# Performance work log

Hardware: AMD Instinct MI355X
Metric: run time of the kernel (lower is better)

Reference implementation:

```python
import jax, jax.numpy as jnp
import numpy as np
from jax import lax

QBITS = 8  # per layer_configs: 8-bit weights and activations


def fake_quant(x, bits=QBITS):
    """Per-tensor symmetric fake quantization with straight-through estimator."""
    qmax = float(2 ** (bits - 1) - 1)  # 127 for 8-bit
    scale = jnp.maximum(jnp.max(jnp.abs(x)), 1e-8) / qmax
    q = jnp.clip(jnp.round(x / scale), -qmax - 1.0, qmax) * scale
    # STE: forward uses q, backward passes gradient through unchanged
    return x + lax.stop_gradient(q - x)


def qconv(x, w, b):
    """Fake-quantized conv: quantize activations and weights, then VALID conv + bias."""
    xq = fake_quant(x)
    wq = fake_quant(w)
    y = lax.conv_general_dilated(
        xq, wq, window_strides=(1, 1), padding='VALID',
        dimension_numbers=('NCHW', 'OIHW', 'NCHW'))
    return y + b[None, :, None, None]


def setup_inputs() -> dict:
    key = jax.random.key(0)
    ks = jax.random.split(key, 9)
    return {
        'x':  jax.random.uniform(ks[0], (256, 1, 128, 128), dtype=jnp.float32),
        'w1': jax.random.normal(ks[1], (16, 1, 3, 3), dtype=jnp.float32) * 0.3,
        'b1': jax.random.normal(ks[2], (16,), dtype=jnp.float32) * 0.05,
        'w2': jax.random.normal(ks[3], (16, 16, 3, 3), dtype=jnp.float32) * 0.1,
        'b2': jax.random.normal(ks[4], (16,), dtype=jnp.float32) * 0.05,
        'w3': jax.random.normal(ks[5], (16, 16, 3, 3), dtype=jnp.float32) * 0.1,
        'b3': jax.random.normal(ks[6], (16,), dtype=jnp.float32) * 0.05,
        'w4': jax.random.normal(ks[7], (1, 16, 2, 2), dtype=jnp.float32) * 0.1,
        'b4': jax.random.normal(ks[8], (1,), dtype=jnp.float32) * 0.05,
    }


def reference(x, w1, b1, w2, b2, w3, b3, w4, b4):
    # x: [N,1,128,128] -> [N,16,126,126] -> [N,16,124,124] -> [N,16,122,122] -> [N,1,121,121]
    h = jax.nn.relu(qconv(x, w1, b1))
    h = jax.nn.relu(qconv(h, w2, b2))
    h = jax.nn.relu(qconv(h, w3, b3))
    return jax.nn.sigmoid(qconv(h, w4, b4))
```

## Files before the change

### kernel.cpp

```cpp
#include <hip/hip_runtime.h>
#include <math.h>


#define THREADS 256

typedef __attribute__((ext_vector_type(4))) int i32x4;

__device__ __forceinline__ int xcd_swz(int bid, int nwg) {
    return (bid & 7) * (nwg >> 3) + (bid >> 3);
}

__device__ __forceinline__ int swzb(int rec) {
    return (rec << 4) ^ ((rec & 56) << 1);
}

__device__ __forceinline__ float block_reduce_max(float m, float* wred) {
#pragma unroll
    for (int off = 32; off > 0; off >>= 1)
        m = fmaxf(m, __shfl_down(m, off, 64));
    if ((threadIdx.x & 63) == 0) wred[threadIdx.x >> 6] = m;
    __syncthreads();
    return fmaxf(fmaxf(wred[0], wred[1]), fmaxf(wred[2], wred[3]));
}

__global__ void init_kernel(unsigned int* slots) {
    if (threadIdx.x < 8) slots[threadIdx.x] = 0u;
}

__global__ void fill_kernel(float* out, int n, float v) {
    int i = blockIdx.x * blockDim.x + threadIdx.x;
    int stride = gridDim.x * blockDim.x;
    for (; i < n; i += stride) out[i] = v;
}

__global__ __launch_bounds__(THREADS) void absmax4_kernel(
    const float4* __restrict__ x, int n4, unsigned int* __restrict__ slot) {
    __shared__ float wred[4];
    float m = 0.f;
    const int stride = gridDim.x * blockDim.x;
    for (int i = blockIdx.x * blockDim.x + threadIdx.x; i < n4; i += stride) {
        float4 v = x[i];
        m = fmaxf(fmaxf(fabsf(v.x), fabsf(v.y)),
                  fmaxf(fmaxf(fabsf(v.z), fabsf(v.w)), m));
    }
    m = block_reduce_max(m, wred);
    if (threadIdx.x == 0) atomicMax(slot, __float_as_uint(m));
}

__global__ __launch_bounds__(THREADS) void quant_w_kernel(
    const float* __restrict__ w1, const float* __restrict__ w2,
    const float* __restrict__ w3, const float* __restrict__ w4,
    float* __restrict__ qw1, float* __restrict__ qw4,
    signed char* __restrict__ wi8_2, signed char* __restrict__ wi8_3,
    unsigned int* __restrict__ slots) {
    __shared__ float wred[4];
    const float* w; int nel;
    switch (blockIdx.x) {
        case 0:  w = w1; nel = 144;  break;
        case 1:  w = w2; nel = 2304; break;
        case 2:  w = w3; nel = 2304; break;
        default: w = w4; nel = 64;   break;
    }
    float m = 0.f;
    for (int i = threadIdx.x; i < nel; i += blockDim.x)
        m = fmaxf(m, fabsf(w[i]));
    m = block_reduce_max(m, wred);
    if (threadIdx.x == 0) slots[4 + blockIdx.x] = __float_as_uint(m);
    const float s = fmaxf(m, 1e-8f) / 127.0f;

    if (blockIdx.x == 0) {
        for (int i = threadIdx.x; i < 144; i += blockDim.x) {
            int p = i % 9, o = i / 9;
            float q = fminf(fmaxf(rintf(w[i] / s), -128.f), 127.f);
            qw1[p * 16 + o] = q * s;
        }
    } else if (blockIdx.x == 3) {
        for (int i = threadIdx.x; i < 64; i += blockDim.x) {
            float q = fminf(fmaxf(rintf(w[i] / s), -128.f), 127.f);
            qw4[i] = q * s;
        }
    } else {
        signed char* wi8 = (blockIdx.x == 1) ? wi8_2 : wi8_3;
        for (int i = threadIdx.x; i < 3072; i += blockDim.x) {
            int ci = i & 15, lane = (i >> 4) & 63, g = i >> 10;
            int co = lane & 15, qq = lane >> 4;
            int pos = 4 * g + qq;
            float v = 0.f;
            if (pos < 9) {
                int ky = pos / 3, kx = pos % 3;
                v = fminf(fmaxf(rintf(w[((co * 16 + ci) * 3 + ky) * 3 + kx] / s),
                                -128.f), 127.f);
            }
            wi8[i] = (signed char)(int)v;
        }
    }
}

template <int MODE>
__global__ __launch_bounds__(THREADS) void conv1_kernel(
    const float* __restrict__ x, const float* __restrict__ qw,
    const float* __restrict__ bias, signed char* __restrict__ out,
    unsigned int* __restrict__ slots) {
    constexpr int IH = 128, IW = 128, OH = 126, OW = 126;
    __shared__ float tile[34 * 34];
    __shared__ float wred[4];
    const int bid = xcd_swz(blockIdx.x, gridDim.x);
    const int n = bid >> 4, tr = bid & 15;
    const int oy0 = (tr >> 2) * 32, ox0 = (tr & 3) * 32;
    const float s_in = fmaxf(__uint_as_float(slots[0]), 1e-8f) / 127.0f;
    const float* xN = x + (size_t)n * IH * IW;

#pragma unroll
    for (int it = 0; it < 5; ++it) {
        int px = it * 256 + threadIdx.x;
        if (px < 1156) {
            int iy = px / 34, ix = px - iy * 34;
            int gy = min(oy0 + iy, IH - 1), gx = min(ox0 + ix, IW - 1);
            float q = rintf(xN[gy * IW + gx] / s_in);
            tile[px] = fminf(fmaxf(q, -128.f), 127.f);
        }
    }
    __syncthreads();

    const int tx = (threadIdx.x & 15) * 2, ty = (threadIdx.x >> 4) * 2;

    float p[4][4];
#pragma unroll
    for (int r = 0; r < 4; ++r) {
        const float* rp = &tile[(ty + r) * 34 + tx];
        p[r][0] = rp[0]; p[r][1] = rp[1]; p[r][2] = rp[2]; p[r][3] = rp[3];
    }

    float r_out = 0.f;
    if constexpr (MODE == 2)
        r_out = 127.0f / fmaxf(__uint_as_float(slots[1]), 1e-8f);

    float accm[16];
#pragma unroll
    for (int c = 0; c < 16; ++c) accm[c] = -3.0e38f;

#pragma unroll
    for (int sy = 0; sy < 2; ++sy)
#pragma unroll
    for (int sx = 0; sx < 2; ++sx) {
        float acc[16];
#pragma unroll
        for (int c = 0; c < 16; ++c) acc[c] = 0.f;
#pragma unroll
        for (int ky = 0; ky < 3; ++ky)
#pragma unroll
        for (int kx = 0; kx < 3; ++kx) {
            const float xv = p[sy + ky][sx + kx];
            const float* wp = qw + (ky * 3 + kx) * 16;
#pragma unroll
            for (int co = 0; co < 16; ++co)
                acc[co] = fmaf(xv, wp[co], acc[co]);
        }
        const int oy = oy0 + ty + sy, ox = ox0 + tx + sx;
        const bool ok = (oy < OH) && (ox < OW);
        if constexpr (MODE == 1) {
            if (ok) {
#pragma unroll
                for (int co = 0; co < 16; ++co)
                    accm[co] = fmaxf(accm[co], acc[co]);
            }
        } else {
            unsigned pk[4] = {0u, 0u, 0u, 0u};
#pragma unroll
            for (int co = 0; co < 16; ++co) {
                float y = fmaxf(fmaf(acc[co], s_in, bias[co]), 0.f);
                float q8 = fminf(rintf(y * r_out), 127.f);
                pk[co >> 2] |= ((unsigned)(int)q8) << ((co & 3) * 8);
            }
            if (ok) {
                int4 v; v.x = pk[0]; v.y = pk[1]; v.z = pk[2]; v.w = pk[3];
                *(int4*)(out + ((size_t)(n * OH + oy) * OW + ox) * 16) = v;
            }
        }
    }
    if constexpr (MODE == 1) {
        float m = 0.f;
#pragma unroll
        for (int co = 0; co < 16; ++co)
            m = fmaxf(m, fmaxf(fmaf(accm[co], s_in, bias[co]), 0.f));
        m = block_reduce_max(m, wred);
        if (threadIdx.x == 0) atomicMax(&slots[1], __float_as_uint(m));
    }
}

template <bool STORE>
__global__ __launch_bounds__(THREADS) void mconv_kernel(
    const signed char* __restrict__ in, const signed char* __restrict__ wi8,
    const float* __restrict__ bias, signed char* __restrict__ out,
    unsigned int* __restrict__ slots, int in_slot, int w_slot, int out_slot,
    int IH, int IW) {
    __shared__ signed char tile[1156 * 16 + 128];
    __shared__ float wred[4];
    const int OH = IH - 2, OW = IW - 2;
    const int bid = xcd_swz(blockIdx.x, gridDim.x);
    const int n = bid >> 4, tr = bid & 15;
    const int oy0 = (tr >> 2) * 32, ox0 = (tr & 3) * 32;

    const int tid = threadIdx.x, lane = tid & 63, wv = tid >> 6;
    const int q = lane >> 4, col = lane & 15;

    const signed char* inN = in + (size_t)n * IH * IW * 16;

#pragma unroll
    for (int it = 0; it < 5; ++it) {
        int px = it * 256 + tid;
        if (px < 1156) {
            int iy = px / 34, ix = px - iy * 34;
            int gy = min(oy0 + iy, IH - 1), gx = min(ox0 + ix, IW - 1);
            *(int4*)(tile + swzb(px)) =
                *(const int4*)(inN + ((size_t)gy * IW + gx) * 16);
        }
    }

    i32x4 afrag[3];
#pragma unroll
    for (int g = 0; g < 3; ++g)
        afrag[g] = ((const i32x4*)wi8)[g * 64 + lane];

    __syncthreads();

    int drec[3];
#pragma unroll
    for (int g = 0; g < 3; ++g) {
        int pos = 4 * g + q;
        int dy = (pos < 9) ? pos / 3 : 0;
        int dx = (pos < 9) ? pos % 3 : 0;
        drec[g] = dy * 34 + dx;
    }
    const int wr = wv >> 1, wc = wv & 1;
    const int bx = 16 * wc + col;
    const int ox = ox0 + bx;

    const float s_in = fmaxf(__uint_as_float(slots[in_slot]), 1e-8f) / 127.0f;
    const float s_w  = fmaxf(__uint_as_float(slots[w_slot]),  1e-8f) / 127.0f;
    const float sxw = s_in * s_w;
    float bj[4];
#pragma unroll
    for (int j = 0; j < 4; ++j) bj[j] = bias[q * 4 + j];
    float r_out = 0.f;
    if constexpr (STORE)
        r_out = 127.0f / fmaxf(__uint_as_float(slots[out_slot]), 1e-8f);

    signed char* outN = out + (size_t)n * OH * OW * 16;
    int mi[4];
#pragma unroll
    for (int j = 0; j < 4; ++j) mi[j] = INT_MIN;

#pragma unroll 4
    for (int r = 0; r < 16; ++r) {
        const int iy = 16 * wr + r;
        const int rec = iy * 34 + bx;
        i32x4 acc = {0, 0, 0, 0};
#pragma unroll
        for (int g = 0; g < 3; ++g) {
            i32x4 b = *(const i32x4*)(tile + swzb(rec + drec[g]));
            acc = __builtin_amdgcn_mfma_i32_16x16x64_i8(afrag[g], b, acc, 0, 0, 0);
        }
        const int oy = oy0 + iy;
        const bool ok = (oy < OH) && (ox < OW);
        if constexpr (STORE) {
            unsigned pk = 0u;
#pragma unroll
            for (int j = 0; j < 4; ++j) {
                float y = fmaxf(fmaf((float)acc[j], sxw, bj[j]), 0.f);
                float q8 = fminf(rintf(y * r_out), 127.f);
                pk |= ((unsigned)(int)q8) << (j * 8);
            }
            if (ok)
                *(unsigned*)(outN + ((size_t)oy * OW + ox) * 16 + q * 4) = pk;
        } else {
            if (ok) {
#pragma unroll
                for (int j = 0; j < 4; ++j)
                    mi[j] = (acc[j] > mi[j]) ? acc[j] : mi[j];
            }
        }
    }
    if constexpr (!STORE) {
        float m = 0.f;
#pragma unroll
        for (int j = 0; j < 4; ++j)
            m = fmaxf(m, fmaxf(fmaf((float)mi[j], sxw, bj[j]), 0.f));
        m = block_reduce_max(m, wred);
        if (tid == 0) atomicMax(&slots[out_slot], __float_as_uint(m));
    }
}

__global__ __launch_bounds__(THREADS) void conv4_kernel(
    const signed char* __restrict__ in, const float* __restrict__ qw,
    const float* __restrict__ bias, float* __restrict__ out,
    unsigned int* __restrict__ slots) {
    constexpr int IH = 122, IW = 122, OH = 121, OW = 121;
    const int bid = xcd_swz(blockIdx.x, gridDim.x);
    const int n = bid >> 4, tr = bid & 15;
    const int oyb = (tr >> 2) * 32 + ((threadIdx.x >> 4) * 2);
    const int oxb = (tr & 3) * 32 + ((threadIdx.x & 15) * 2);
    const float s_in = fmaxf(__uint_as_float(slots[3]), 1e-8f) / 127.0f;
    const float b0 = bias[0];
    const signed char* inN = in + (size_t)n * IH * IW * 16;

    float w[64];
#pragma unroll
    for (int i = 0; i < 64; ++i) w[i] = qw[i];

#pragma unroll
    for (int sy = 0; sy < 2; ++sy)
#pragma unroll
    for (int sx = 0; sx < 2; ++sx) {
        const int oy = oyb + sy, ox = oxb + sx;
        if (oy >= OH || ox >= OW) continue;
        float acc = 0.f;
#pragma unroll
        for (int ky = 0; ky < 2; ++ky)
#pragma unroll
        for (int kx = 0; kx < 2; ++kx) {
            union { int4 v; signed char c[16]; } u;
            u.v = *(const int4*)(inN + ((size_t)(oy + ky) * IW + ox + kx) * 16);
#pragma unroll
            for (int ci = 0; ci < 16; ++ci)
                acc = fmaf((float)u.c[ci], w[(ci * 2 + ky) * 2 + kx], acc);
        }
        float y = fmaf(acc, s_in, b0);
        out[(size_t)(n * OH + oy) * OW + ox] = 1.0f / (1.0f + expf(-y));
    }
}

extern "C" void kernel_launch(void* const* d_in, const int* in_sizes, int n_in,
                              void* d_out, int out_size, void* d_ws, size_t ws_size,
                              hipStream_t stream) {
    (void)in_sizes; (void)n_in;
    const float* x  = (const float*)d_in[0];
    const float* w1 = (const float*)d_in[1];
    const float* b1 = (const float*)d_in[2];
    const float* w2 = (const float*)d_in[3];
    const float* b2 = (const float*)d_in[4];
    const float* w3 = (const float*)d_in[5];
    const float* b3 = (const float*)d_in[6];
    const float* w4 = (const float*)d_in[7];
    const float* b4 = (const float*)d_in[8];

    char* ws = (char*)d_ws;
    unsigned int* slots = (unsigned int*)ws;
    float* qw1 = (float*)(ws + 256);
    float* qw4 = (float*)(ws + 1024);
    signed char* wi8_2 = (signed char*)(ws + 2048);
    signed char* wi8_3 = (signed char*)(ws + 5120);

    const size_t Q1 = 65028096ULL;
    const size_t Q2 = 62980096ULL;
    signed char* qb1 = (signed char*)(ws + 32768);
    signed char* qb2 = (signed char*)(ws + 32768 + Q1);
    float* outp = (float*)d_out;

    const size_t need = 32768ULL + Q1 + Q2;
    if (ws_size < need) {
        float v = 100.0f + (float)(ws_size >> 20);
        hipLaunchKernelGGL(fill_kernel, dim3(1024), dim3(THREADS), 0, stream,
                           outp, out_size, v);
        return;
    }

    const int blocks = 256 * 16;

    hipLaunchKernelGGL(init_kernel, dim3(1), dim3(64), 0, stream, slots);
    hipLaunchKernelGGL(absmax4_kernel, dim3(2048), dim3(THREADS), 0, stream,
                       (const float4*)x, 256 * 128 * 128 / 4, slots + 0);
    hipLaunchKernelGGL(quant_w_kernel, dim3(4), dim3(THREADS), 0, stream,
                       w1, w2, w3, w4, qw1, qw4, wi8_2, wi8_3, slots);

    hipLaunchKernelGGL((conv1_kernel<1>), dim3(blocks), dim3(THREADS), 0, stream,
                       x, qw1, b1, nullptr, slots);
    hipLaunchKernelGGL((conv1_kernel<2>), dim3(blocks), dim3(THREADS), 0, stream,
                       x, qw1, b1, qb1, slots);
    hipLaunchKernelGGL((mconv_kernel<false>), dim3(blocks), dim3(THREADS), 0, stream,
                       qb1, wi8_2, b2, nullptr, slots, 1, 5, 2, 126, 126);
    hipLaunchKernelGGL((mconv_kernel<true>), dim3(blocks), dim3(THREADS), 0, stream,
                       qb1, wi8_2, b2, qb2, slots, 1, 5, 2, 126, 126);
    hipLaunchKernelGGL((mconv_kernel<false>), dim3(blocks), dim3(THREADS), 0, stream,
                       qb2, wi8_3, b3, nullptr, slots, 2, 6, 3, 124, 124);
    hipLaunchKernelGGL((mconv_kernel<true>), dim3(blocks), dim3(THREADS), 0, stream,
                       qb2, wi8_3, b3, qb1, slots, 2, 6, 3, 124, 124);
    hipLaunchKernelGGL(conv4_kernel, dim3(blocks), dim3(THREADS), 0, stream,
                       qb1, qw4, b4, outp, slots);
}
```

Measured before the change: 333.5 us.

## Fuse adjacent conv stages with halo tiles to cut kernel launches and intermediate traffic

Replaces the seven-pass schedule (a max pass and a store pass per layer) with four kernels. Each kernel computes one layer's quantized output into shared memory and immediately runs the next layer's max-reduction or convolution on it. Tiles shrink to 30x30 outputs with overlapping halos, giving 25 tiles per image. This removes several full reads of the int8 intermediates and the separate conv4 pass. In exchange, halo work is recomputed, shared memory per block grows, and fewer blocks may fit per CU.

```diff
diff --git a/kernel.cpp b/kernel.cpp
--- a/kernel.cpp
+++ b/kernel.cpp
@@ -9,7 +9,6 @@
 __device__ __forceinline__ int xcd_swz(int bid, int nwg) {
     return (bid & 7) * (nwg >> 3) + (bid >> 3);
 }
-
 __device__ __forceinline__ int swzb(int rec) {
     return (rec << 4) ^ ((rec & 56) << 1);
 }
@@ -96,11 +95,9 @@
     }
 }
 
-template <int MODE>
-__global__ __launch_bounds__(THREADS) void conv1_kernel(
+__global__ __launch_bounds__(THREADS) void conv1max_kernel(
     const float* __restrict__ x, const float* __restrict__ qw,
-    const float* __restrict__ bias, signed char* __restrict__ out,
-    unsigned int* __restrict__ slots) {
+    const float* __restrict__ bias, unsigned int* __restrict__ slots) {
     constexpr int IH = 128, IW = 128, OH = 126, OW = 126;
     __shared__ float tile[34 * 34];
     __shared__ float wred[4];
@@ -123,18 +120,12 @@
     __syncthreads();
 
     const int tx = (threadIdx.x & 15) * 2, ty = (threadIdx.x >> 4) * 2;
-
     float p[4][4];
 #pragma unroll
     for (int r = 0; r < 4; ++r) {
         const float* rp = &tile[(ty + r) * 34 + tx];
         p[r][0] = rp[0]; p[r][1] = rp[1]; p[r][2] = rp[2]; p[r][3] = rp[3];
     }
-
-    float r_out = 0.f;
-    if constexpr (MODE == 2)
-        r_out = 127.0f / fmaxf(__uint_as_float(slots[1]), 1e-8f);
-
     float accm[16];
 #pragma unroll
     for (int c = 0; c < 16; ++c) accm[c] = -3.0e38f;
@@ -157,73 +148,83 @@
                 acc[co] = fmaf(xv, wp[co], acc[co]);
         }
         const int oy = oy0 + ty + sy, ox = ox0 + tx + sx;
-        const bool ok = (oy < OH) && (ox < OW);
-        if constexpr (MODE == 1) {
-            if (ok) {
-#pragma unroll
-                for (int co = 0; co < 16; ++co)
-                    accm[co] = fmaxf(accm[co], acc[co]);
-            }
-        } else {
-            unsigned pk[4] = {0u, 0u, 0u, 0u};
-#pragma unroll
-            for (int co = 0; co < 16; ++co) {
-                float y = fmaxf(fmaf(acc[co], s_in, bias[co]), 0.f);
-                float q8 = fminf(rintf(y * r_out), 127.f);
-                pk[co >> 2] |= ((unsigned)(int)q8) << ((co & 3) * 8);
-            }
-            if (ok) {
-                int4 v; v.x = pk[0]; v.y = pk[1]; v.z = pk[2]; v.w = pk[3];
-                *(int4*)(out + ((size_t)(n * OH + oy) * OW + ox) * 16) = v;
-            }
-        }
-    }
-    if constexpr (MODE == 1) {
-        float m = 0.f;
-#pragma unroll
-        for (int co = 0; co < 16; ++co)
-            m = fmaxf(m, fmaxf(fmaf(accm[co], s_in, bias[co]), 0.f));
-        m = block_reduce_max(m, wred);
-        if (threadIdx.x == 0) atomicMax(&slots[1], __float_as_uint(m));
-    }
-}
-
-template <bool STORE>
-__global__ __launch_bounds__(THREADS) void mconv_kernel(
-    const signed char* __restrict__ in, const signed char* __restrict__ wi8,
-    const float* __restrict__ bias, signed char* __restrict__ out,
-    unsigned int* __restrict__ slots, int in_slot, int w_slot, int out_slot,
-    int IH, int IW) {
-    __shared__ signed char tile[1156 * 16 + 128];
+        if (oy < OH && ox < OW) {
+#pragma unroll
+            for (int co = 0; co < 16; ++co)
+                accm[co] = fmaxf(accm[co], acc[co]);
+        }
+    }
+    float m = 0.f;
+#pragma unroll
+    for (int co = 0; co < 16; ++co)
+        m = fmaxf(m, fmaxf(fmaf(accm[co], s_in, bias[co]), 0.f));
+    m = block_reduce_max(m, wred);
+    if (threadIdx.x == 0) atomicMax(&slots[1], __float_as_uint(m));
+}
+
+__global__ __launch_bounds__(THREADS) void k3_kernel(
+    const float* __restrict__ x, const float* __restrict__ qw1,
+    const float* __restrict__ b1, signed char* __restrict__ h1out,
+    const signed char* __restrict__ wi8_2, const float* __restrict__ b2,
+    unsigned int* __restrict__ slots) {
+    __shared__ float xt[36 * 36];
+    __shared__ signed char h1t[34 * 34 * 16 + 128];
     __shared__ float wred[4];
-    const int OH = IH - 2, OW = IW - 2;
     const int bid = xcd_swz(blockIdx.x, gridDim.x);
-    const int n = bid >> 4, tr = bid & 15;
-    const int oy0 = (tr >> 2) * 32, ox0 = (tr & 3) * 32;
-
-    const int tid = threadIdx.x, lane = tid & 63, wv = tid >> 6;
+    const int n = bid / 25, tr = bid % 25;
+    const int ty = (tr / 5) * 30, tx = (tr % 5) * 30;
+    const int tid = threadIdx.x;
+
+    const float s_x = fmaxf(__uint_as_float(slots[0]), 1e-8f) / 127.0f;
+    const float r1  = 127.0f / fmaxf(__uint_as_float(slots[1]), 1e-8f);
+    const float* xN = x + (size_t)n * 128 * 128;
+
+    for (int i = tid; i < 1296; i += THREADS) {
+        int iy = i / 36, ix = i - iy * 36;
+        int gy = min(ty + iy, 127), gx = min(tx + ix, 127);
+        float q = rintf(xN[gy * 128 + gx] / s_x);
+        xt[i] = fminf(fmaxf(q, -128.f), 127.f);
+    }
+    __syncthreads();
+
+    for (int p = tid; p < 1156; p += THREADS) {
+        int py = p / 34, px = p - py * 34;
+        float acc[16];
+#pragma unroll
+        for (int c = 0; c < 16; ++c) acc[c] = 0.f;
+#pragma unroll
+        for (int ky = 0; ky < 3; ++ky)
+#pragma unroll
+        for (int kx = 0; kx < 3; ++kx) {
+            const float xv = xt[(py + ky) * 36 + px + kx];
+            const float* wp = qw1 + (ky * 3 + kx) * 16;
+#pragma unroll
+            for (int co = 0; co < 16; ++co)
+                acc[co] = fmaf(xv, wp[co], acc[co]);
+        }
+        unsigned pk[4] = {0u, 0u, 0u, 0u};
+#pragma unroll
+        for (int co = 0; co < 16; ++co) {
+            float y = fmaxf(fmaf(acc[co], s_x, b1[co]), 0.f);
+            float q8 = fminf(rintf(y * r1), 127.f);
+            pk[co >> 2] |= ((unsigned)(int)q8) << ((co & 3) * 8);
+        }
+        int4 v; v.x = pk[0]; v.y = pk[1]; v.z = pk[2]; v.w = pk[3];
+        *(int4*)(h1t + swzb(p)) = v;
+        const int gy = ty + py, gx = tx + px;
+        if (gy <= 125 && gx <= 125)
+            *(int4*)(h1out + ((size_t)(n * 126 + gy) * 126 + gx) * 16) = v;
+    }
+
+    i32x4 afrag[3];
+#pragma unroll
+    for (int g = 0; g < 3; ++g)
+        afrag[g] = ((const i32x4*)wi8_2)[g * 64 + (tid & 63)];
+    __syncthreads();
+
+    const int lane = tid & 63, wv = tid >> 6;
     const int q = lane >> 4, col = lane & 15;
-
-    const signed char* inN = in + (size_t)n * IH * IW * 16;
-
-#pragma unroll
-    for (int it = 0; it < 5; ++it) {
-        int px = it * 256 + tid;
-        if (px < 1156) {
-            int iy = px / 34, ix = px - iy * 34;
-            int gy = min(oy0 + iy, IH - 1), gx = min(ox0 + ix, IW - 1);
-            *(int4*)(tile + swzb(px)) =
-                *(const int4*)(inN + ((size_t)gy * IW + gx) * 16);
-        }
-    }
-
-    i32x4 afrag[3];
-#pragma unroll
-    for (int g = 0; g < 3; ++g)
-        afrag[g] = ((const i32x4*)wi8)[g * 64 + lane];
-
-    __syncthreads();
-
+    const int wr = wv >> 1, wc = wv & 1;
     int drec[3];
 #pragma unroll
     for (int g = 0; g < 3; ++g) {
@@ -232,101 +233,246 @@
         int dx = (pos < 9) ? pos % 3 : 0;
         drec[g] = dy * 34 + dx;
     }
-    const int wr = wv >> 1, wc = wv & 1;
-    const int bx = 16 * wc + col;
-    const int ox = ox0 + bx;
-
-    const float s_in = fmaxf(__uint_as_float(slots[in_slot]), 1e-8f) / 127.0f;
-    const float s_w  = fmaxf(__uint_as_float(slots[w_slot]),  1e-8f) / 127.0f;
-    const float sxw = s_in * s_w;
-    float bj[4];
-#pragma unroll
-    for (int j = 0; j < 4; ++j) bj[j] = bias[q * 4 + j];
-    float r_out = 0.f;
-    if constexpr (STORE)
-        r_out = 127.0f / fmaxf(__uint_as_float(slots[out_slot]), 1e-8f);
-
-    signed char* outN = out + (size_t)n * OH * OW * 16;
+    const int ix2 = 16 * wc + col;
     int mi[4];
 #pragma unroll
     for (int j = 0; j < 4; ++j) mi[j] = INT_MIN;
 
 #pragma unroll 4
     for (int r = 0; r < 16; ++r) {
-        const int iy = 16 * wr + r;
-        const int rec = iy * 34 + bx;
+        const int iy2 = 16 * wr + r;
+        const int rec = iy2 * 34 + ix2;
         i32x4 acc = {0, 0, 0, 0};
 #pragma unroll
         for (int g = 0; g < 3; ++g) {
-            i32x4 b = *(const i32x4*)(tile + swzb(rec + drec[g]));
+            i32x4 b = *(const i32x4*)(h1t + swzb(rec + drec[g]));
             acc = __builtin_amdgcn_mfma_i32_16x16x64_i8(afrag[g], b, acc, 0, 0, 0);
         }
-        const int oy = oy0 + iy;
-        const bool ok = (oy < OH) && (ox < OW);
-        if constexpr (STORE) {
-            unsigned pk = 0u;
-#pragma unroll
-            for (int j = 0; j < 4; ++j) {
-                float y = fmaxf(fmaf((float)acc[j], sxw, bj[j]), 0.f);
-                float q8 = fminf(rintf(y * r_out), 127.f);
-                pk |= ((unsigned)(int)q8) << (j * 8);
+        if (ty + iy2 <= 123 && tx + ix2 <= 123) {
+#pragma unroll
+            for (int j = 0; j < 4; ++j)
+                mi[j] = (acc[j] > mi[j]) ? acc[j] : mi[j];
+        }
+    }
+    const float s1  = fmaxf(__uint_as_float(slots[1]), 1e-8f) / 127.0f;
+    const float sw2 = fmaxf(__uint_as_float(slots[5]), 1e-8f) / 127.0f;
+    const float sxw = s1 * sw2;
+    float m = 0.f;
+#pragma unroll
+    for (int j = 0; j < 4; ++j)
+        m = fmaxf(m, fmaxf(fmaf((float)mi[j], sxw, b2[q * 4 + j]), 0.f));
+    m = block_reduce_max(m, wred);
+    if (tid == 0) atomicMax(&slots[2], __float_as_uint(m));
+}
+
+__global__ __launch_bounds__(THREADS) void k4_kernel(
+    const signed char* __restrict__ h1, const signed char* __restrict__ wi8_2,
+    const float* __restrict__ b2, signed char* __restrict__ h2out,
+    const signed char* __restrict__ wi8_3, const float* __restrict__ b3,
+    unsigned int* __restrict__ slots) {
+    __shared__ signed char h1t[34 * 34 * 16 + 128];
+    __shared__ signed char h2t[32 * 32 * 16 + 128];
+    __shared__ float wred[4];
+    const int bid = xcd_swz(blockIdx.x, gridDim.x);
+    const int n = bid / 25, tr = bid % 25;
+    const int ty = (tr / 5) * 30, tx = (tr % 5) * 30;
+    const int tid = threadIdx.x, lane = tid & 63, wv = tid >> 6;
+    const int q = lane >> 4, col = lane & 15;
+    const int wr = wv >> 1, wc = wv & 1;
+
+    const signed char* h1N = h1 + (size_t)n * 126 * 126 * 16;
+#pragma unroll
+    for (int it = 0; it < 5; ++it) {
+        int p = it * 256 + tid;
+        if (p < 1156) {
+            int iy = p / 34, ix = p - iy * 34;
+            int gy = min(ty + iy, 125), gx = min(tx + ix, 125);
+            *(int4*)(h1t + swzb(p)) =
+                *(const int4*)(h1N + ((size_t)gy * 126 + gx) * 16);
+        }
+    }
+    i32x4 af2[3], af3[3];
+#pragma unroll
+    for (int g = 0; g < 3; ++g) {
+        af2[g] = ((const i32x4*)wi8_2)[g * 64 + lane];
+        af3[g] = ((const i32x4*)wi8_3)[g * 64 + lane];
+    }
+    __syncthreads();
+
+    int d34[3], d32[3];
+#pragma unroll
+    for (int g = 0; g < 3; ++g) {
+        int pos = 4 * g + q;
+        int dy = (pos < 9) ? pos / 3 : 0;
+        int dx = (pos < 9) ? pos % 3 : 0;
+        d34[g] = dy * 34 + dx;
+        d32[g] = dy * 32 + dx;
+    }
+    const float s1  = fmaxf(__uint_as_float(slots[1]), 1e-8f) / 127.0f;
+    const float sw2 = fmaxf(__uint_as_float(slots[5]), 1e-8f) / 127.0f;
+    const float sxw2 = s1 * sw2;
+    const float r2 = 127.0f / fmaxf(__uint_as_float(slots[2]), 1e-8f);
+    float b2j[4];
+#pragma unroll
+    for (int j = 0; j < 4; ++j) b2j[j] = b2[q * 4 + j];
+
+    const int ix2 = 16 * wc + col;
+    signed char* h2N = h2out + (size_t)n * 124 * 124 * 16;
+
+#pragma unroll 4
+    for (int r = 0; r < 16; ++r) {
+        const int iy2 = 16 * wr + r;
+        const int rec = iy2 * 34 + ix2;
+        i32x4 acc = {0, 0, 0, 0};
+#pragma unroll
+        for (int g = 0; g < 3; ++g) {
+            i32x4 b = *(const i32x4*)(h1t + swzb(rec + d34[g]));
+            acc = __builtin_amdgcn_mfma_i32_16x16x64_i8(af2[g], b, acc, 0, 0, 0);
+        }
+        unsigned pk = 0u;
+#pragma unroll
+        for (int j = 0; j < 4; ++j) {
+            float y = fmaxf(fmaf((float)acc[j], sxw2, b2j[j]), 0.f);
+            float q8 = fminf(rintf(y * r2), 127.f);
+            pk |= ((unsigned)(int)q8) << (j * 8);
+        }
+        *(unsigned*)(h2t + swzb(iy2 * 32 + ix2) + q * 4) = pk;
+        const int gy = ty + iy2, gx = tx + ix2;
+        if (gy <= 123 && gx <= 123)
+            *(unsigned*)(h2N + ((size_t)gy * 124 + gx) * 16 + q * 4) = pk;
+    }
+    __syncthreads();
+
+    int mi[4];
+#pragma unroll
+    for (int j = 0; j < 4; ++j) mi[j] = INT_MIN;
+#pragma unroll 4
+    for (int r = 0; r < 16; ++r) {
+        const int iy3 = 16 * wr + r;
+        if (iy3 <= 29) {
+            const int rec = iy3 * 32 + ix2;
+            i32x4 acc = {0, 0, 0, 0};
+#pragma unroll
+            for (int g = 0; g < 3; ++g) {
+                i32x4 b = *(const i32x4*)(h2t + swzb(rec + d32[g]));
+                acc = __builtin_amdgcn_mfma_i32_16x16x64_i8(af3[g], b, acc, 0, 0, 0);
             }
-            if (ok)
-                *(unsigned*)(outN + ((size_t)oy * OW + ox) * 16 + q * 4) = pk;
-        } else {
-            if (ok) {
+            if (ix2 <= 29 && ty + iy3 <= 121 && tx + ix2 <= 121) {
 #pragma unroll
                 for (int j = 0; j < 4; ++j)
                     mi[j] = (acc[j] > mi[j]) ? acc[j] : mi[j];
             }
         }
     }
-    if constexpr (!STORE) {
-        float m = 0.f;
-#pragma unroll
-        for (int j = 0; j < 4; ++j)
-            m = fmaxf(m, fmaxf(fmaf((float)mi[j], sxw, bj[j]), 0.f));
-        m = block_reduce_max(m, wred);
-        if (tid == 0) atomicMax(&slots[out_slot], __float_as_uint(m));
-    }
-}
-
-__global__ __launch_bounds__(THREADS) void conv4_kernel(
-    const signed char* __restrict__ in, const float* __restrict__ qw,
-    const float* __restrict__ bias, float* __restrict__ out,
+    const float s2  = fmaxf(__uint_as_float(slots[2]), 1e-8f) / 127.0f;
+    const float sw3 = fmaxf(__uint_as_float(slots[6]), 1e-8f) / 127.0f;
+    const float sxw3 = s2 * sw3;
+    float m = 0.f;
+#pragma unroll
+    for (int j = 0; j < 4; ++j)
+        m = fmaxf(m, fmaxf(fmaf((float)mi[j], sxw3, b3[q * 4 + j]), 0.f));
+    m = block_reduce_max(m, wred);
+    if (tid == 0) atomicMax(&slots[3], __float_as_uint(m));
+}
+
+__global__ __launch_bounds__(THREADS) void k5_kernel(
+    const signed char* __restrict__ h2, const signed char* __restrict__ wi8_3,
+    const float* __restrict__ b3, const float* __restrict__ qw4,
+    const float* __restrict__ b4, float* __restrict__ out,
     unsigned int* __restrict__ slots) {
-    constexpr int IH = 122, IW = 122, OH = 121, OW = 121;
+    __shared__ signed char h2t[34 * 34 * 16 + 128];
+    __shared__ signed char h3t[32 * 32 * 16 + 128];
     const int bid = xcd_swz(blockIdx.x, gridDim.x);
-    const int n = bid >> 4, tr = bid & 15;
-    const int oyb = (tr >> 2) * 32 + ((threadIdx.x >> 4) * 2);
-    const int oxb = (tr & 3) * 32 + ((threadIdx.x & 15) * 2);
-    const float s_in = fmaxf(__uint_as_float(slots[3]), 1e-8f) / 127.0f;
-    const float b0 = bias[0];
-    const signed char* inN = in + (size_t)n * IH * IW * 16;
-
+    const int n = bid / 25, tr = bid % 25;
+    const int ty = (tr / 5) * 30, tx = (tr % 5) * 30;
+    const int tid = threadIdx.x, lane = tid & 63, wv = tid >> 6;
+    const int q = lane >> 4, col = lane & 15;
+    const int wr = wv >> 1, wc = wv & 1;
+
+    const signed char* h2N = h2 + (size_t)n * 124 * 124 * 16;
+#pragma unroll
+    for (int it = 0; it < 5; ++it) {
+        int p = it * 256 + tid;
+        if (p < 1156) {
+            int iy = p / 34, ix = p - iy * 34;
+            int gy = min(ty + iy, 123), gx = min(tx + ix, 123);
+            *(int4*)(h2t + swzb(p)) =
+                *(const int4*)(h2N + ((size_t)gy * 124 + gx) * 16);
+        }
+    }
+    i32x4 af3[3];
+#pragma unroll
+    for (int g = 0; g < 3; ++g)
+        af3[g] = ((const i32x4*)wi8_3)[g * 64 + lane];
+    __syncthreads();
+
+    int d34[3];
+#pragma unroll
+    for (int g = 0; g < 3; ++g) {
+        int pos = 4 * g + q;
+        int dy = (pos < 9) ? pos / 3 : 0;
+        int dx = (pos < 9) ? pos % 3 : 0;
+        d34[g] = dy * 34 + dx;
+    }
+    const float s2  = fmaxf(__uint_as_float(slots[2]), 1e-8f) / 127.0f;
+    const float sw3 = fmaxf(__uint_as_float(slots[6]), 1e-8f) / 127.0f;
+    const float sxw3 = s2 * sw3;
+    const float r3 = 127.0f / fmaxf(__uint_as_float(slots[3]), 1e-8f);
+    float b3j[4];
+#pragma unroll
+    for (int j = 0; j < 4; ++j) b3j[j] = b3[q * 4 + j];
+    const int ix3 = 16 * wc + col;
+
+#pragma unroll 4
+    for (int r = 0; r < 16; ++r) {
+        const int iy3 = 16 * wr + r;
+        const int rec = iy3 * 34 + ix3;
+        i32x4 acc = {0, 0, 0, 0};
+#pragma unroll
+        for (int g = 0; g < 3; ++g) {
+            i32x4 b = *(const i32x4*)(h2t + swzb(rec + d34[g]));
+            acc = __builtin_amdgcn_mfma_i32_16x16x64_i8(af3[g], b, acc, 0, 0, 0);
+        }
+        unsigned pk = 0u;
+#pragma unroll
+        for (int j = 0; j < 4; ++j) {
+            float y = fmaxf(fmaf((float)acc[j], sxw3, b3j[j]), 0.f);
+            float q8 = fminf(rintf(y * r3), 127.f);
+            pk |= ((unsigned)(int)q8) << (j * 8);
+        }
+        *(unsigned*)(h3t + swzb(iy3 * 32 + ix3) + q * 4) = pk;
+    }
+    __syncthreads();
+
+    const float s3 = fmaxf(__uint_as_float(slots[3]), 1e-8f) / 127.0f;
+    const float bb = b4[0];
     float w[64];
 #pragma unroll
-    for (int i = 0; i < 64; ++i) w[i] = qw[i];
-
-#pragma unroll
-    for (int sy = 0; sy < 2; ++sy)
-#pragma unroll
-    for (int sx = 0; sx < 2; ++sx) {
-        const int oy = oyb + sy, ox = oxb + sx;
-        if (oy >= OH || ox >= OW) continue;
-        float acc = 0.f;
-#pragma unroll
-        for (int ky = 0; ky < 2; ++ky)
-#pragma unroll
-        for (int kx = 0; kx < 2; ++kx) {
-            union { int4 v; signed char c[16]; } u;
-            u.v = *(const int4*)(inN + ((size_t)(oy + ky) * IW + ox + kx) * 16);
-#pragma unroll
-            for (int ci = 0; ci < 16; ++ci)
-                acc = fmaf((float)u.c[ci], w[(ci * 2 + ky) * 2 + kx], acc);
-        }
-        float y = fmaf(acc, s_in, b0);
-        out[(size_t)(n * OH + oy) * OW + ox] = 1.0f / (1.0f + expf(-y));
+    for (int i = 0; i < 64; ++i) w[i] = qw4[i];
+    float* outN = out + (size_t)n * 121 * 121;
+
+#pragma unroll
+    for (int it = 0; it < 4; ++it) {
+        int p = it * 256 + tid;
+        if (p < 961) {
+            int r = p / 31, c = p - r * 31;
+            float acc = 0.f;
+#pragma unroll
+            for (int ky = 0; ky < 2; ++ky)
+#pragma unroll
+            for (int kx = 0; kx < 2; ++kx) {
+                union { int4 v; signed char ch[16]; } u;
+                u.v = *(const int4*)(h3t + swzb((r + ky) * 32 + (c + kx)));
+#pragma unroll
+                for (int ci = 0; ci < 16; ++ci)
+                    acc = fmaf((float)u.ch[ci], w[(ci * 2 + ky) * 2 + kx], acc);
+            }
+            const int gy = ty + r, gx = tx + c;
+            if (gy <= 120 && gx <= 120) {
+                float y = fmaf(acc, s3, bb);
+                outN[(size_t)gy * 121 + gx] = 1.0f / (1.0f + expf(-y));
+            }
+        }
     }
 }
 
@@ -365,26 +511,19 @@
         return;
     }
 
-    const int blocks = 256 * 16;
-
     hipLaunchKernelGGL(init_kernel, dim3(1), dim3(64), 0, stream, slots);
     hipLaunchKernelGGL(absmax4_kernel, dim3(2048), dim3(THREADS), 0, stream,
                        (const float4*)x, 256 * 128 * 128 / 4, slots + 0);
     hipLaunchKernelGGL(quant_w_kernel, dim3(4), dim3(THREADS), 0, stream,
                        w1, w2, w3, w4, qw1, qw4, wi8_2, wi8_3, slots);
 
-    hipLaunchKernelGGL((conv1_kernel<1>), dim3(blocks), dim3(THREADS), 0, stream,
-                       x, qw1, b1, nullptr, slots);
-    hipLaunchKernelGGL((conv1_kernel<2>), dim3(blocks), dim3(THREADS), 0, stream,
-                       x, qw1, b1, qb1, slots);
-    hipLaunchKernelGGL((mconv_kernel<false>), dim3(blocks), dim3(THREADS), 0, stream,
-                       qb1, wi8_2, b2, nullptr, slots, 1, 5, 2, 126, 126);
-    hipLaunchKernelGGL((mconv_kernel<true>), dim3(blocks), dim3(THREADS), 0, stream,
-                       qb1, wi8_2, b2, qb2, slots, 1, 5, 2, 126, 126);
-    hipLaunchKernelGGL((mconv_kernel<false>), dim3(blocks), dim3(THREADS), 0, stream,
-                       qb2, wi8_3, b3, nullptr, slots, 2, 6, 3, 124, 124);
-    hipLaunchKernelGGL((mconv_kernel<true>), dim3(blocks), dim3(THREADS), 0, stream,
-                       qb2, wi8_3, b3, qb1, slots, 2, 6, 3, 124, 124);
-    hipLaunchKernelGGL(conv4_kernel, dim3(blocks), dim3(THREADS), 0, stream,
-                       qb1, qw4, b4, outp, slots);
-}
+    hipLaunchKernelGGL(conv1max_kernel, dim3(256 * 16), dim3(THREADS), 0, stream,
+                       x, qw1, b1, slots);
+    const int fgrid = 256 * 25;
+    hipLaunchKernelGGL(k3_kernel, dim3(fgrid), dim3(THREADS), 0, stream,
+                       x, qw1, b1, qb1, wi8_2, b2, slots);
+    hipLaunchKernelGGL(k4_kernel, dim3(fgrid), dim3(THREADS), 0, stream,
+                       qb1, wi8_2, b2, qb2, wi8_3, b3, slots);
+    hipLaunchKernelGGL(k5_kernel, dim3(fgrid), dim3(THREADS), 0, stream,
+                       qb2, wi8_3, b3, qw4, b4, outp, slots);
+}
```

New measurement: 363.3 us. +9.0%, slower.
